# Kernel optimization log

Hardware: AMD Instinct MI355X
Metric: run time of the kernel (lower is better)

Reference implementation:

```python
import jax, jax.numpy as jnp
import numpy as np

DIM = 512
HEADS = 8
SCALE = (DIM // HEADS) ** -0.5  # 0.125
B, H, W = 1, 64, 64  # square spatial grid required by torch matmul broadcasting


def setup_inputs() -> dict:
    key = jax.random.key(0)
    ks = jax.random.split(key, 7)
    s = DIM ** -0.5
    return {
        "x": jax.random.normal(ks[0], (B, H, W, DIM), dtype=jnp.float32),
        "mask": 0,  # sentinel for None (mask must be None in the original)
        "Wq": jax.random.normal(ks[1], (DIM, DIM), dtype=jnp.float32) * s,
        "bq": jax.random.normal(ks[2], (DIM,), dtype=jnp.float32) * 0.01,
        "Wk": jax.random.normal(ks[3], (DIM, DIM), dtype=jnp.float32) * s,
        "bk": jax.random.normal(ks[4], (DIM,), dtype=jnp.float32) * 0.01,
        "Wv": jax.random.normal(ks[5], (DIM, DIM), dtype=jnp.float32) * s,
        "bv": jax.random.normal(ks[6], (DIM,), dtype=jnp.float32) * 0.01,
    }


def reference(x, mask, Wq, bq, Wk, bk, Wv, bv):
    # Linear projections (nn.Linear: x @ W.T + b)
    q = jnp.einsum('bhwc,oc->bhwo', x, Wq) + bq
    k = jnp.einsum('bhwc,oc->bhwo', x, Wk) + bk
    v = jnp.einsum('bhwc,oc->bhwo', x, Wv) + bv
    # Faithful to torch.einsum('bhwc,bpqd->bhwpq', q, k): c and d are each
    # summed independently => outer product of channel-sums. [b,h,w,p,q]
    weights = jnp.einsum('bhwc,bpqd->bhwpq', q, k)
    # dropout is identity in eval mode; then scale and softmax over last axis
    weights = jax.nn.softmax(weights * SCALE, axis=-1)
    # torch matmul broadcasting: [b,h,w,p,q] @ [b,p,q,d] -> [b,h,w,p,d]
    attn = jnp.matmul(weights, v)
    return attn
```

## Files before the change

kernel.cpp:

```cpp
#include <hip/hip_runtime.h>

typedef _Float16 half8 __attribute__((ext_vector_type(8)));
typedef float f32x4 __attribute__((ext_vector_type(4)));
typedef float float4_t __attribute__((ext_vector_type(4)));
typedef unsigned int uint32x2 __attribute__((ext_vector_type(2)));

#define DIM 512
#define S 64
#define NROW 4096
#define LDSW 88

__device__ __forceinline__ void bar_lds() {
    asm volatile("s_waitcnt lgkmcnt(0)" ::: "memory");
    __builtin_amdgcn_s_barrier();
    asm volatile("" ::: "memory");
}

__global__ void colsum2_kernel(const float* __restrict__ Wq, const float* __restrict__ bq,
                               const float* __restrict__ Wk, const float* __restrict__ bk,
                               float* __restrict__ wsumq, float* __restrict__ wsumk) {
    int sel = blockIdx.x >> 5;
    int b = blockIdx.x & 31;
    const float* W = sel ? Wk : Wq;
    const float* bias = sel ? bk : bq;
    float* wsum = sel ? wsumk : wsumq;
    int t = threadIdx.x;
    int c0 = t, c1 = t + 256;
    float s0 = 0.f, s1 = 0.f;
    const float* Wr = W + (size_t)b * 16 * DIM;
#pragma unroll
    for (int o = 0; o < 16; ++o) {
        s0 += Wr[o * DIM + c0];
        s1 += Wr[o * DIM + c1];
    }
    atomicAdd(&wsum[c0], s0);
    atomicAdd(&wsum[c1], s1);
    if (b == 0) {
        float bs = bias[c0] + bias[c1];
#pragma unroll
        for (int off = 32; off >= 1; off >>= 1) bs += __shfl_xor(bs, off);
        if ((t & 63) == 0) atomicAdd(&wsum[512], bs);
    }
}

__global__ void rowdot_vt_kernel(const float* __restrict__ X,
                                 const float* __restrict__ wqsum,
                                 const float* __restrict__ wksum,
                                 float* __restrict__ a_arr,
                                 float* __restrict__ ks_arr,
                                 const float* __restrict__ Wv,
                                 const float* __restrict__ bv,
                                 _Float16* __restrict__ Vs) {
    int bid = blockIdx.x;
    if (bid < 1024) {
        int wave = threadIdx.x >> 6;
        int lane = threadIdx.x & 63;
        int row = bid * 4 + wave;
        const float4_t* xr = (const float4_t*)(X + (size_t)row * DIM) + lane * 2;
        const float4_t* wq = (const float4_t*)wqsum + lane * 2;
        const float4_t* wk = (const float4_t*)wksum + lane * 2;
        float4_t x0 = xr[0], x1 = xr[1];
        float4_t q0 = wq[0], q1 = wq[1];
        float4_t k0 = wk[0], k1 = wk[1];
        float sq = 0.f, sk = 0.f;
#pragma unroll
        for (int i = 0; i < 4; i++) {
            sq += x0[i] * q0[i] + x1[i] * q1[i];
            sk += x0[i] * k0[i] + x1[i] * k1[i];
        }
#pragma unroll
        for (int off = 32; off >= 1; off >>= 1) {
            sq += __shfl_xor(sq, off);
            sk += __shfl_xor(sk, off);
        }
        if (lane == 0) {
            a_arr[row]  = (sq + wqsum[DIM]) * 0.125f;
            ks_arr[row] = sk + wksum[DIM];
        }
        return;
    }
    int b2 = bid - 1024;
    int mb = b2 & 255;
    int cb = b2 >> 8;
    int wv_ = threadIdx.x >> 6;
    int lane = threadIdx.x & 63;
    int lr = lane & 15;
    int lg = lane >> 4;
    int row0 = mb * 16;
    int col0 = cb * 256 + wv_ * 64;

    f32x4 acc[4];
#pragma unroll
    for (int n = 0; n < 4; n++) acc[n] = (f32x4){0.f, 0.f, 0.f, 0.f};

    for (int kk = 0; kk < 16; ++kk) {
        int kbase = kk * 32 + lg * 8;
        const float4_t* pa = (const float4_t*)(X + (size_t)(row0 + lr) * DIM + kbase);
        float4_t x0 = pa[0], x1 = pa[1];
        half8 a;
#pragma unroll
        for (int i = 0; i < 4; i++) { a[i] = (_Float16)x0[i]; a[i + 4] = (_Float16)x1[i]; }
#pragma unroll
        for (int n = 0; n < 4; n++) {
            const float4_t* pb = (const float4_t*)(Wv + (size_t)(col0 + n * 16 + lr) * DIM + kbase);
            float4_t b0 = pb[0], b1 = pb[1];
            half8 hb;
#pragma unroll
            for (int i = 0; i < 4; i++) { hb[i] = (_Float16)b0[i]; hb[i + 4] = (_Float16)b1[i]; }
            acc[n] = __builtin_amdgcn_mfma_f32_16x16x32_f16(a, hb, acc[n], 0, 0, 0);
        }
    }
    int w   = mb >> 2;
    int s_  = (mb & 3) >> 1;
    int lg2 = ((mb & 3) * 2 + (lg >> 1)) & 3;
    int e0  = (lg & 1) * 4;
#pragma unroll
    for (int n = 0; n < 4; n++) {
        int d = col0 + n * 16 + lr;
        int dt = d >> 4;
        float bvc = bv[d];
        _Float16 tmp[4];
#pragma unroll
        for (int r = 0; r < 4; r++) tmp[r] = (_Float16)(acc[n][r] + bvc);
        int idx8 = (((w * 32 + dt) * 2 + s_) * 4 + lg2) * 16 + lr;
        __builtin_nontemporal_store(*(uint32x2*)tmp, (uint32x2*)(Vs + (size_t)idx8 * 8 + e0));
    }
}

__global__ __launch_bounds__(256) void attn_main_kernel(
        const float* __restrict__ a_arr,
        const float* __restrict__ ks_arr,
        const _Float16* __restrict__ Vs,
        float* __restrict__ out) {
    __shared__ _Float16 Wsm[64 * LDSW];
    __shared__ float Osm[64 * 128];
    int hw = blockIdx.x;
    int w = hw & 63;
    int t = threadIdx.x;
    int wv_ = t >> 6, lane = t & 63;
    int lr = lane & 15, lg = lane >> 4;

    const half8* Vg = (const half8*)Vs;

    int dtb = wv_ * 2;
    half8 vc0 = Vg[((w * 32 + dtb) * 2 + 0) * 64 + lane];
    half8 vc1 = Vg[((w * 32 + dtb) * 2 + 1) * 64 + lane];
    half8 vc2 = Vg[((w * 32 + dtb + 1) * 2 + 0) * 64 + lane];
    half8 vc3 = Vg[((w * 32 + dtb + 1) * 2 + 1) * 64 + lane];

    float a = a_arr[hw];

    {
        int p = t >> 2, c = t & 3;
        const float4_t* kp = (const float4_t*)(ks_arr + p * 64 + c * 16);
        float4_t k0 = kp[0], k1 = kp[1], k2 = kp[2], k3 = kp[3];
        float L[16];
#pragma unroll
        for (int i = 0; i < 4; i++) {
            L[i] = a * k0[i]; L[4 + i] = a * k1[i];
            L[8 + i] = a * k2[i]; L[12 + i] = a * k3[i];
        }
        float m = L[0];
#pragma unroll
        for (int i = 1; i < 16; i++) m = fmaxf(m, L[i]);
        m = fmaxf(m, __shfl_xor(m, 1));
        m = fmaxf(m, __shfl_xor(m, 2));
        float e[16];
        float sum = 0.f;
#pragma unroll
        for (int i = 0; i < 16; i++) { e[i] = __expf(L[i] - m); sum += e[i]; }
        sum += __shfl_xor(sum, 1);
        sum += __shfl_xor(sum, 2);
        float r = 1.0f / sum;
        half8 h0, h1;
#pragma unroll
        for (int i = 0; i < 8; i++) {
            h0[i] = (_Float16)(e[i] * r);
            h1[i] = (_Float16)(e[8 + i] * r);
        }
        *(half8*)&Wsm[p * LDSW + c * 16]     = h0;
        *(half8*)&Wsm[p * LDSW + c * 16 + 8] = h1;
    }
    bar_lds();

    half8 wfr[4][2];
#pragma unroll
    for (int pt = 0; pt < 4; ++pt)
#pragma unroll
        for (int s_ = 0; s_ < 2; ++s_)
            wfr[pt][s_] = *(const half8*)&Wsm[(pt * 16 + lr) * LDSW + s_ * 32 + lg * 8];

    char* outb = (char*)(out + (size_t)hw * (64 * DIM));

#pragma unroll
    for (int j2 = 0; j2 < 4; ++j2) {
        half8 vn0, vn1, vn2, vn3;
        if (j2 < 3) {
            int dt0 = (j2 + 1) * 8 + dtb;
            vn0 = Vg[((w * 32 + dt0) * 2 + 0) * 64 + lane];
            vn1 = Vg[((w * 32 + dt0) * 2 + 1) * 64 + lane];
            vn2 = Vg[((w * 32 + dt0 + 1) * 2 + 0) * 64 + lane];
            vn3 = Vg[((w * 32 + dt0 + 1) * 2 + 1) * 64 + lane];
        }
        f32x4 acc[2][4];
#pragma unroll
        for (int c = 0; c < 2; ++c)
#pragma unroll
            for (int pt = 0; pt < 4; ++pt) acc[c][pt] = (f32x4){0.f, 0.f, 0.f, 0.f};
#pragma unroll
        for (int pt = 0; pt < 4; ++pt) {
            acc[0][pt] = __builtin_amdgcn_mfma_f32_16x16x32_f16(vc0, wfr[pt][0], acc[0][pt], 0, 0, 0);
            acc[0][pt] = __builtin_amdgcn_mfma_f32_16x16x32_f16(vc1, wfr[pt][1], acc[0][pt], 0, 0, 0);
            acc[1][pt] = __builtin_amdgcn_mfma_f32_16x16x32_f16(vc2, wfr[pt][0], acc[1][pt], 0, 0, 0);
            acc[1][pt] = __builtin_amdgcn_mfma_f32_16x16x32_f16(vc3, wfr[pt][1], acc[1][pt], 0, 0, 0);
        }
        bar_lds();
#pragma unroll
        for (int c = 0; c < 2; ++c)
#pragma unroll
            for (int pt = 0; pt < 4; ++pt) {
                int p = pt * 16 + lr;
                int addr = p * 512 + (wv_ * 32 + c * 16 + lg * 4) * 4;
                addr ^= (p & 7) << 4;
                *(f32x4*)((char*)Osm + addr) = acc[c][pt];
            }
        bar_lds();
#pragma unroll
        for (int i = 0; i < 8; ++i) {
            int f = i * 4096 + t * 16;
            int row = f >> 9;
            int rb = f ^ ((row & 7) << 4);
            f32x4 val = *(const f32x4*)((const char*)Osm + rb);
            __builtin_nontemporal_store(val, (f32x4*)(outb + (size_t)row * 2048 + j2 * 512 + (f & 511)));
        }
        vc0 = vn0; vc1 = vn1; vc2 = vn2; vc3 = vn3;
    }
}

extern "C" void kernel_launch(void* const* d_in, const int* in_sizes, int n_in,
                              void* d_out, int out_size, void* d_ws, size_t ws_size,
                              hipStream_t stream) {
    const float* x  = (const float*)d_in[0];
    const float* Wq = (const float*)d_in[2];
    const float* bq = (const float*)d_in[3];
    const float* Wk = (const float*)d_in[4];
    const float* bk = (const float*)d_in[5];
    const float* Wv = (const float*)d_in[6];
    const float* bv = (const float*)d_in[7];
    float* out = (float*)d_out;
    char* ws = (char*)d_ws;

    _Float16* Vs  = (_Float16*)ws;
    float* a_arr  = (float*)(ws + 4194304);
    float* ks_arr = (float*)(ws + 4210688);
    float* wqsum  = (float*)(ws + 4227072);
    float* wksum  = (float*)(ws + 4229184);

    hipMemsetAsync(ws + 4227072, 0, 4224, stream);
    colsum2_kernel<<<64, 256, 0, stream>>>(Wq, bq, Wk, bk, wqsum, wksum);
    rowdot_vt_kernel<<<1536, 256, 0, stream>>>(x, wqsum, wksum, a_arr, ks_arr, Wv, bv, Vs);
    attn_main_kernel<<<4096, 256, 0, stream>>>(a_arr, ks_arr, Vs, out);
}
```

Baseline: 147.7 us.

## Restructure attention output loop by p-tile with full-row contiguous stores

The main kernel now preloads all V fragments for its wave (8 d-tiles) up front and loops over four p-tiles instead of four d-chunks. Each iteration writes full contiguous 32 KB output rows with regular stores rather than strided nontemporal stores. The Wsm and Osm shared arrays are aliased into one 32 KB buffer, and launch bounds request 3 waves per EU. The colsum kernel is split over 256 blocks instead of 64. This trades more live VGPRs for V against a more contiguous write pattern and lower LDS use, so occupancy could drop.

```diff
diff --git a/kernel.cpp b/kernel.cpp
--- a/kernel.cpp
+++ b/kernel.cpp
@@ -19,17 +19,17 @@
 __global__ void colsum2_kernel(const float* __restrict__ Wq, const float* __restrict__ bq,
                                const float* __restrict__ Wk, const float* __restrict__ bk,
                                float* __restrict__ wsumq, float* __restrict__ wsumk) {
-    int sel = blockIdx.x >> 5;
-    int b = blockIdx.x & 31;
+    int sel = blockIdx.x >> 7;
+    int b = blockIdx.x & 127;
     const float* W = sel ? Wk : Wq;
     const float* bias = sel ? bk : bq;
     float* wsum = sel ? wsumk : wsumq;
     int t = threadIdx.x;
     int c0 = t, c1 = t + 256;
     float s0 = 0.f, s1 = 0.f;
-    const float* Wr = W + (size_t)b * 16 * DIM;
-#pragma unroll
-    for (int o = 0; o < 16; ++o) {
+    const float* Wr = W + (size_t)b * 4 * DIM;
+#pragma unroll
+    for (int o = 0; o < 4; ++o) {
         s0 += Wr[o * DIM + c0];
         s1 += Wr[o * DIM + c1];
     }
@@ -127,13 +127,15 @@
     }
 }
 
-__global__ __launch_bounds__(256) void attn_main_kernel(
+__global__ __launch_bounds__(256, 3) void attn_main_kernel(
         const float* __restrict__ a_arr,
         const float* __restrict__ ks_arr,
         const _Float16* __restrict__ Vs,
         float* __restrict__ out) {
-    __shared__ _Float16 Wsm[64 * LDSW];
-    __shared__ float Osm[64 * 128];
+    __shared__ __align__(16) char smem[32768];
+    _Float16* Wsm = (_Float16*)smem;
+    char* Osm = smem;
+
     int hw = blockIdx.x;
     int w = hw & 63;
     int t = threadIdx.x;
@@ -142,11 +144,14 @@
 
     const half8* Vg = (const half8*)Vs;
 
-    int dtb = wv_ * 2;
-    half8 vc0 = Vg[((w * 32 + dtb) * 2 + 0) * 64 + lane];
-    half8 vc1 = Vg[((w * 32 + dtb) * 2 + 1) * 64 + lane];
-    half8 vc2 = Vg[((w * 32 + dtb + 1) * 2 + 0) * 64 + lane];
-    half8 vc3 = Vg[((w * 32 + dtb + 1) * 2 + 1) * 64 + lane];
+    half8 vfr[8][2];
+#pragma unroll
+    for (int j = 0; j < 8; ++j) {
+        int dt = wv_ * 8 + j;
+        int g0 = ((w * 32 + dt) * 2) * 64 + lane;
+        vfr[j][0] = Vg[g0];
+        vfr[j][1] = Vg[g0 + 64];
+    }
 
     float a = a_arr[hw];
 
@@ -193,47 +198,32 @@
     char* outb = (char*)(out + (size_t)hw * (64 * DIM));
 
 #pragma unroll
-    for (int j2 = 0; j2 < 4; ++j2) {
-        half8 vn0, vn1, vn2, vn3;
-        if (j2 < 3) {
-            int dt0 = (j2 + 1) * 8 + dtb;
-            vn0 = Vg[((w * 32 + dt0) * 2 + 0) * 64 + lane];
-            vn1 = Vg[((w * 32 + dt0) * 2 + 1) * 64 + lane];
-            vn2 = Vg[((w * 32 + dt0 + 1) * 2 + 0) * 64 + lane];
-            vn3 = Vg[((w * 32 + dt0 + 1) * 2 + 1) * 64 + lane];
-        }
-        f32x4 acc[2][4];
-#pragma unroll
-        for (int c = 0; c < 2; ++c)
-#pragma unroll
-            for (int pt = 0; pt < 4; ++pt) acc[c][pt] = (f32x4){0.f, 0.f, 0.f, 0.f};
-#pragma unroll
-        for (int pt = 0; pt < 4; ++pt) {
-            acc[0][pt] = __builtin_amdgcn_mfma_f32_16x16x32_f16(vc0, wfr[pt][0], acc[0][pt], 0, 0, 0);
-            acc[0][pt] = __builtin_amdgcn_mfma_f32_16x16x32_f16(vc1, wfr[pt][1], acc[0][pt], 0, 0, 0);
-            acc[1][pt] = __builtin_amdgcn_mfma_f32_16x16x32_f16(vc2, wfr[pt][0], acc[1][pt], 0, 0, 0);
-            acc[1][pt] = __builtin_amdgcn_mfma_f32_16x16x32_f16(vc3, wfr[pt][1], acc[1][pt], 0, 0, 0);
+    for (int pt = 0; pt < 4; ++pt) {
+        f32x4 acc[8];
+#pragma unroll
+        for (int j = 0; j < 8; ++j) acc[j] = (f32x4){0.f, 0.f, 0.f, 0.f};
+#pragma unroll
+        for (int j = 0; j < 8; ++j) {
+            acc[j] = __builtin_amdgcn_mfma_f32_16x16x32_f16(vfr[j][0], wfr[pt][0], acc[j], 0, 0, 0);
+            acc[j] = __builtin_amdgcn_mfma_f32_16x16x32_f16(vfr[j][1], wfr[pt][1], acc[j], 0, 0, 0);
         }
         bar_lds();
 #pragma unroll
-        for (int c = 0; c < 2; ++c)
-#pragma unroll
-            for (int pt = 0; pt < 4; ++pt) {
-                int p = pt * 16 + lr;
-                int addr = p * 512 + (wv_ * 32 + c * 16 + lg * 4) * 4;
-                addr ^= (p & 7) << 4;
-                *(f32x4*)((char*)Osm + addr) = acc[c][pt];
-            }
+        for (int j = 0; j < 8; ++j) {
+            int d = wv_ * 128 + j * 16 + lg * 4;
+            int addr = lr * 2048 + d * 4;
+            addr ^= (lr & 7) << 4;
+            *(f32x4*)(Osm + addr) = acc[j];
+        }
         bar_lds();
 #pragma unroll
         for (int i = 0; i < 8; ++i) {
             int f = i * 4096 + t * 16;
-            int row = f >> 9;
-            int rb = f ^ ((row & 7) << 4);
-            f32x4 val = *(const f32x4*)((const char*)Osm + rb);
-            __builtin_nontemporal_store(val, (f32x4*)(outb + (size_t)row * 2048 + j2 * 512 + (f & 511)));
-        }
-        vc0 = vn0; vc1 = vn1; vc2 = vn2; vc3 = vn3;
+            int p = f >> 11;
+            int rb = f ^ ((p & 7) << 4);
+            f32x4 val = *(const f32x4*)(Osm + rb);
+            *(f32x4*)(outb + pt * 32768 + f) = val;
+        }
     }
 }
 
@@ -257,7 +247,7 @@
     float* wksum  = (float*)(ws + 4229184);
 
     hipMemsetAsync(ws + 4227072, 0, 4224, stream);
-    colsum2_kernel<<<64, 256, 0, stream>>>(Wq, bq, Wk, bk, wqsum, wksum);
+    colsum2_kernel<<<256, 256, 0, stream>>>(Wq, bq, Wk, bk, wqsum, wksum);
     rowdot_vt_kernel<<<1536, 256, 0, stream>>>(x, wqsum, wksum, a_arr, ks_arr, Wv, bv, Vs);
     attn_main_kernel<<<4096, 256, 0, stream>>>(a_arr, ks_arr, Vs, out);
 }
```

Measured after the change: 153.2 us. 1.04x slower.
